# Kernel optimization log

Measured on AMD Instinct MI355X. Metric: run time of the kernel, lower is better.

The kernel has to match this reference:

```python
import math
import jax, jax.numpy as jnp
import numpy as np

B, M, N, D, H = 64, 5, 1000, 128, 8
KS = D // H
TANH_CLIP = 10.0

def setup_inputs() -> dict:
    key = jax.random.key(0)
    ks = jax.random.split(key, 12)
    mask = jax.random.randint(ks[8], (B, M, N), 0, 2).astype(bool)
    mask = mask.at[:, 0, 0].set(True)  # guarantee at least one feasible action per batch row
    return {
        'node_embeddings': jax.random.normal(ks[0], (B, N, D), jnp.float32),
        'fixed_context': jax.random.normal(ks[1], (B, 1, D), jnp.float32),
        'prev_node_embeddings': jax.random.normal(ks[2], (B, M, D), jnp.float32),
        'node_dynamic_features': jax.random.normal(ks[3], (B, M, N, 8), jnp.float32),
        'vehicle_dynamic_features': jax.random.normal(ks[4], (B, M, 3), jnp.float32),
        'glimpse_V_static': jax.random.normal(ks[5], (H, B, 1, N, KS), jnp.float32),
        'glimpse_K_static': jax.random.normal(ks[6], (H, B, 1, N, KS), jnp.float32),
        'logit_K_static': jax.random.normal(ks[7], (B, 1, N, D), jnp.float32),
        'feasibility_mask': mask,
        'W_pcv': jax.random.normal(ks[9], (D, D + 3), jnp.float32) * 0.05,
        'W_pns': jax.random.normal(ks[10], (3 * D, 8), jnp.float32) * 0.05,
        'po_weight': jax.random.normal(ks[11], (D, D), jnp.float32) * 0.05,
    }

def reference(node_embeddings, fixed_context, prev_node_embeddings,
              node_dynamic_features, vehicle_dynamic_features,
              glimpse_V_static, glimpse_K_static, logit_K_static,
              feasibility_mask, W_pcv, W_pns, po_weight):
    # current vehicle state projection: [B,M,D]
    cvs = jnp.concatenate([prev_node_embeddings, vehicle_dynamic_features], axis=-1)
    proj_cvs = cvs @ W_pcv.T
    # dynamic node embeddings: [B,M,N,3D] -> three [B,M,N,D] chunks
    nde = node_dynamic_features @ W_pns.T
    gVd, gKd, lKd = jnp.split(nde, 3, axis=-1)
    # make heads: [B,M,N,D] -> [H,B,M,N,KS]
    def mh(x):
        return x.reshape(B, M, N, H, KS).transpose(3, 0, 1, 2, 4)
    glimpse_V = glimpse_V_static + mh(gVd)  # [H,B,M,N,KS]
    glimpse_K = glimpse_K_static + mh(gKd)
    logit_K = logit_K_static + lKd          # [B,M,N,D]
    query = fixed_context + proj_cvs        # [B,M,D]
    Q = query.reshape(B, M, H, KS).transpose(2, 0, 1, 3)  # [H,B,M,KS]
    mask_log = jnp.log(feasibility_mask.astype(jnp.float32))  # [B,M,N]
    compat = jnp.einsum('hbmk,hbmnk->hbmn', Q, glimpse_K) / math.sqrt(KS)
    compat = compat + mask_log[None]
    # softmax over joint vehicle*node axis
    attn = jax.nn.softmax(compat.reshape(H, B, M * N), axis=-1).reshape(H, B, M, N)
    heads = jnp.einsum('hbmn,hbmnk->hbmk', attn, glimpse_V)  # [H,B,M,KS]
    concat = heads.transpose(1, 2, 0, 3).reshape(B, M, D)
    final_Q = concat @ po_weight.T          # [B,M,D]
    logits = jnp.einsum('bmd,bmnd->bmn', final_Q, logit_K) / math.sqrt(D)
    logits = jnp.tanh(logits) * TANH_CLIP + mask_log
    probs = jax.nn.softmax(logits.reshape(B, M * N), axis=-1)
    return probs
```

## Files before the change

### kernel.cpp

```cpp
#include <hip/hip_runtime.h>
#include <cstddef>

#define BB 64
#define MM 5
#define NN 1000
#define DD 128
#define HH 8
#define KSZ 16
#define NT 8
#define TN 125
#define NC3 8
#define CH3 125
#define INV_SQRT_D 0.08838834764831845f

#define K2_KOFF 0
#define K2_VOFF 8192
#define K2_NOFF 16384
#define K2_POFF 36864
#define K2_BUF  37376

typedef __attribute__((address_space(1))) const void gconst_t;
typedef __attribute__((address_space(3))) void lds_t;
#define GLD16(src, dst) __builtin_amdgcn_global_load_lds((gconst_t*)(src), (lds_t*)(dst), 16, 0, 0)
#define GLD4(src, dst)  __builtin_amdgcn_global_load_lds((gconst_t*)(src), (lds_t*)(dst), 4, 0, 0)
#define VMCNT0() asm volatile("s_waitcnt vmcnt(0)" ::: "memory")

__device__ __forceinline__ float tanh_fast(float x) {
  float e = __expf(2.f * x);
  return 1.f - 2.f / (e + 1.f);
}

__global__ __launch_bounds__(256) void k1_query(
    const float* __restrict__ fc, const float* __restrict__ pne,
    const float* __restrict__ vdf, const float* __restrict__ wpcv,
    const float* __restrict__ wpns, const int* __restrict__ mask,
    float* __restrict__ q_ws, float* __restrict__ qw_ws,
    unsigned int* __restrict__ pmask)
{
  const int t = threadIdx.x;
  if (blockIdx.x >= BB * 4) {
    const int b = blockIdx.x - BB * 4;
    const int* mb = mask + (size_t)(b * MM) * NN;
    for (int n = t; n < NN; n += 256) {
      unsigned int pm = 0;
#pragma unroll
      for (int m = 0; m < MM; ++m) pm |= (mb[m * NN + n] != 0 ? 1u : 0u) << m;
      pmask[b * NN + n] = pm;
    }
    return;
  }
  const int b = blockIdx.x >> 2;
  const int dq = blockIdx.x & 3;
  const int k = t & 15, gid = t >> 4;
  __shared__ float qsh[MM][32];

  float cvr[9];
  int curm = -1;
  for (int r = 0; r < 10; ++r) {
    const int m = r >> 1;
    if (m != curm) {
      curm = m;
      const float* pner = pne + (size_t)(b * MM + m) * DD;
#pragma unroll
      for (int jp = 0; jp < 8; ++jp) cvr[jp] = pner[k + 16 * jp];
      cvr[8] = (k < 3) ? vdf[(b * MM + m) * 3 + k] : 0.f;
    }
    const int dl = (r & 1) * 16 + gid;
    const int d = dq * 32 + dl;
    const float* wrow = wpcv + d * 131;
    float p = 0.f;
#pragma unroll
    for (int jp = 0; jp < 8; ++jp) p = fmaf(cvr[jp], wrow[k + 16 * jp], p);
    if (k < 3) p = fmaf(cvr[8], wrow[128 + k], p);
    p += __shfl_xor(p, 1); p += __shfl_xor(p, 2);
    p += __shfl_xor(p, 4); p += __shfl_xor(p, 8);
    if (k == 0) {
      const float q = 0.25f * (p + fc[b * DD + d]);
      qsh[m][dl] = q;
      q_ws[(size_t)(b * MM + m) * DD + d] = q;
    }
  }
  __syncthreads();
  if (t < 80) {
    const int hh = t / 40;
    const int r = t - hh * 40, m = r >> 3, f = r & 7;
    const int h = dq * 2 + hh;
    float acc = 0.f;
#pragma unroll
    for (int kk = 0; kk < KSZ; ++kk)
      acc = fmaf(qsh[m][hh * 16 + kk], wpns[(DD + h * KSZ + kk) * 8 + f], acc);
    qw_ws[(b * HH + h) * 40 + m * 8 + f] = acc;
  }
}

__global__ __launch_bounds__(256, 2) void k2_attn(
    const float* __restrict__ ndf, const float* __restrict__ gV,
    const float* __restrict__ gK, const unsigned int* __restrict__ pmask,
    const float* __restrict__ q_ws, const float* __restrict__ qw_ws,
    float* __restrict__ part)
{
  const int bid = blockIdx.x;
  const int b = bid & 63;
  const int h = bid >> 6;
  const int t = threadIdx.x;
  const int w = t >> 6, lane = t & 63;
  const int k = t & 3, g = t >> 2;

  __shared__ __align__(16) char smem[2][K2_BUF];
  __shared__ float redh[4][MM][KSZ];
  __shared__ float redaf[4][MM][8];
  __shared__ float reds[4];

  const char* gkrow = (const char*)gK + (size_t)(h * BB + b) * (NN * 64);
  const char* gvrow = (const char*)gV + (size_t)(h * BB + b) * (NN * 64);
  const char* pmrow = (const char*)pmask + (size_t)b * (NN * 4);
  const char* ndrow0 = (const char*)ndf + (size_t)(b * MM) * (NN * 32);

  auto stage = [&](int tt, int bb) {
    char* base = smem[bb];
#pragma unroll
    for (int j = 0; j < 10; ++j) {
      const int seg = 4 * j + w;
      if (seg >= 38) continue;
      if (seg < 16) {
        const int s = seg & 7;
        int off = tt * 8000 + s * 1024;
        if (off > NN * 64 - 1024) off = NN * 64 - 1024;
        const char* srow = (seg < 8) ? gkrow : gvrow;
        const int roff = (seg < 8) ? K2_KOFF : K2_VOFF;
        GLD16(srow + off + lane * 16, base + roff + (off - tt * 8000));
      } else if (seg < 36) {
        const int rel = seg - 16, m = rel >> 2, q = rel & 3;
        int off = tt * 4000 + q * 1024;
        if (off > NN * 32 - 1024) off = NN * 32 - 1024;
        GLD16(ndrow0 + (size_t)m * (NN * 32) + off + lane * 16,
              base + K2_NOFF + m * 4096 + (off - tt * 4000));
      } else {
        const int i4 = seg - 36;
        int off = tt * 500 + i4 * 256;
        if (off > NN * 4 - 256) off = NN * 4 - 256;
        GLD4(pmrow + off + lane * 4, base + K2_POFF + (off - tt * 500));
      }
    }
  };

  float4 qr[MM];
  float2 qw[MM];
#pragma unroll
  for (int m = 0; m < MM; ++m) {
    qr[m] = *(const float4*)(q_ws + (size_t)(b * MM + m) * DD + h * KSZ + 4 * k);
    qw[m] = *(const float2*)(qw_ws + (b * HH + h) * 40 + m * 8 + 2 * k);
  }

  float4 ha[MM] = {};
  float2 af[MM] = {};
  float ls = 0.f;

  stage(0, 0);
  VMCNT0();
  __builtin_amdgcn_s_barrier();

  for (int tt = 0; tt < NT; ++tt) {
    const int cur = tt & 1;
    if (tt < NT - 1) stage(tt + 1, cur ^ 1);
    const char* base = smem[cur];
#pragma unroll
    for (int i = 0; i < 2; ++i) {
      const int n = g + 64 * i;
      if (i == 0 || g < TN - 64) {
        const float4 kv = *(const float4*)(base + K2_KOFF + n * 64 + k * 16);
        const float4 vv = *(const float4*)(base + K2_VOFF + n * 64 + k * 16);
        const unsigned int pm = *(const unsigned int*)(base + K2_POFF + n * 4);
        float2 nd[MM];
#pragma unroll
        for (int m = 0; m < MM; ++m)
          nd[m] = *(const float2*)(base + K2_NOFF + m * 4096 + n * 32 + k * 8);
#pragma unroll
        for (int m = 0; m < MM; ++m) {
          float p = kv.x * qr[m].x + kv.y * qr[m].y
                  + kv.z * qr[m].z + kv.w * qr[m].w
                  + nd[m].x * qw[m].x + nd[m].y * qw[m].y;
          p += __shfl_xor(p, 1); p += __shfl_xor(p, 2);
          const float e = ((pm >> m) & 1u) ? __expf(p) : 0.f;
          ha[m].x = fmaf(e, vv.x, ha[m].x);
          ha[m].y = fmaf(e, vv.y, ha[m].y);
          ha[m].z = fmaf(e, vv.z, ha[m].z);
          ha[m].w = fmaf(e, vv.w, ha[m].w);
          af[m].x = fmaf(e, nd[m].x, af[m].x);
          af[m].y = fmaf(e, nd[m].y, af[m].y);
          ls += e;
        }
      }
    }
    VMCNT0();
    __builtin_amdgcn_s_barrier();
  }

#pragma unroll
  for (int off = 4; off <= 32; off <<= 1) {
#pragma unroll
    for (int m = 0; m < MM; ++m) {
      ha[m].x += __shfl_xor(ha[m].x, off);
      ha[m].y += __shfl_xor(ha[m].y, off);
      ha[m].z += __shfl_xor(ha[m].z, off);
      ha[m].w += __shfl_xor(ha[m].w, off);
      af[m].x += __shfl_xor(af[m].x, off);
      af[m].y += __shfl_xor(af[m].y, off);
    }
    ls += __shfl_xor(ls, off);
  }
  if (lane < 4) {
#pragma unroll
    for (int m = 0; m < MM; ++m) {
      *(float4*)(&redh[w][m][4 * k]) = ha[m];
      *(float2*)(&redaf[w][m][2 * k]) = af[m];
    }
    if (k == 0) reds[w] = ls;
  }
  __syncthreads();
  float* P = part + (size_t)(b * HH + h) * 128;
  if (t < 80) {
    const int m = t >> 4, kk = t & 15;
    P[t] = redh[0][m][kk] + redh[1][m][kk] + redh[2][m][kk] + redh[3][m][kk];
  } else if (t < 120) {
    const int r = t - 80, m = r >> 3, f = r & 7;
    P[80 + r] = redaf[0][m][f] + redaf[1][m][f] + redaf[2][m][f] + redaf[3][m][f];
  } else if (t == 120) {
    P[120] = reds[0] + reds[1] + reds[2] + reds[3];
  }
}

__global__ __launch_bounds__(512) void k3_logits(
    const float* __restrict__ ndf, const float* __restrict__ lK,
    const unsigned int* __restrict__ pmask, const float* __restrict__ part,
    const float* __restrict__ wpns, const float* __restrict__ po,
    float* __restrict__ out, float* __restrict__ stats)
{
  const int b = blockIdx.x >> 3;
  const int c = blockIdx.x & 7;
  const int t = threadIdx.x;

  __shared__ float pos[DD][129];
  __shared__ float rgs[HH];
  __shared__ float afs[HH][MM][8];
  __shared__ float cs[MM][DD];
  __shared__ float fqs[MM][DD];
  __shared__ float fw[MM][8];
  __shared__ float wred[8];

  for (int i = t; i < DD * DD / 4; i += 512) {
    const float4 v = ((const float4*)po)[i];
    const int r = (i * 4) >> 7, cc = (i * 4) & 127;
    pos[r][cc] = v.x; pos[r][cc + 1] = v.y; pos[r][cc + 2] = v.z; pos[r][cc + 3] = v.w;
  }
  const float* pb = part + (size_t)b * HH * 128;
  if (t < HH) rgs[t] = 1.f / pb[t * 128 + 120];
  if (t < HH * MM * 8) {
    const int h = t / 40, r = t % 40;
    afs[h][r >> 3][r & 7] = pb[h * 128 + 80 + r];
  }
  __syncthreads();
  for (int idx = t; idx < MM * DD; idx += 512) {
    const int m = idx >> 7, d = idx & 127, h = d >> 4;
    const float a = pb[h * 128 + m * 16 + (d & 15)];
    float cf = 0.f;
#pragma unroll
    for (int f = 0; f < 8; ++f) cf = fmaf(wpns[d * 8 + f], afs[h][m][f], cf);
    cs[m][d] = (a + cf) * rgs[h];
  }
  __syncthreads();
  for (int idx = t; idx < MM * DD; idx += 512) {
    const int m = idx >> 7, d = idx & 127;
    float acc = 0.f;
#pragma unroll 8
    for (int j = 0; j < DD; ++j) acc = fmaf(cs[m][j], pos[d][j], acc);
    fqs[m][d] = acc * INV_SQRT_D;
  }
  __syncthreads();
  if (t < MM * 8) {
    const int m = t >> 3, f = t & 7;
    float acc = 0.f;
#pragma unroll 16
    for (int d = 0; d < DD; ++d) acc = fmaf(fqs[m][d], wpns[(2 * DD + d) * 8 + f], acc);
    fw[m][f] = acc;
  }
  __syncthreads();

  const int k = t & 15, gid = t >> 4;
  const int n0 = c * CH3;
  float4 fqr[MM][2];
  float fwr[MM];
#pragma unroll
  for (int m = 0; m < MM; ++m) {
    fqr[m][0] = *(const float4*)(&fqs[m][8 * k]);
    fqr[m][1] = *(const float4*)(&fqs[m][8 * k + 4]);
    fwr[m] = fw[m][k & 7];
  }
  float lsum = 0.f;

#pragma unroll
  for (int i = 0; i < 4; ++i) {
    const int nl = gid + 32 * i;
    const bool valid = (nl < CH3);
    const int n = n0 + (valid ? nl : 0);
    const unsigned int pm = valid ? pmask[b * NN + n] : 0u;
    const float* lkr = lK + ((size_t)b * NN + n) * DD;
    const float4 l0 = *(const float4*)(lkr + 8 * k);
    const float4 l1 = *(const float4*)(lkr + 8 * k + 4);
    float ndv[MM];
#pragma unroll
    for (int m = 0; m < MM; ++m)
      ndv[m] = (k < 8) ? ndf[((size_t)(b * MM + m) * NN + n) * 8 + k] : 0.f;
#pragma unroll
    for (int m = 0; m < MM; ++m) {
      float p = l0.x * fqr[m][0].x + l0.y * fqr[m][0].y
              + l0.z * fqr[m][0].z + l0.w * fqr[m][0].w
              + l1.x * fqr[m][1].x + l1.y * fqr[m][1].y
              + l1.z * fqr[m][1].z + l1.w * fqr[m][1].w
              + ndv[m] * fwr[m];
      p += __shfl_xor(p, 1); p += __shfl_xor(p, 2);
      p += __shfl_xor(p, 4); p += __shfl_xor(p, 8);
      const float e = ((pm >> m) & 1u) ? __expf(tanh_fast(p) * 10.f) : 0.f;
      if (valid) {
        lsum += e;
        if (k == 0) out[(size_t)(b * MM + m) * NN + n] = e;
      }
    }
  }
  lsum += __shfl_xor(lsum, 16);
  lsum += __shfl_xor(lsum, 32);
  if ((t & 63) == 0) wred[t >> 6] = lsum;
  __syncthreads();
  if (t == 0) {
    float s = 0.f;
#pragma unroll
    for (int w2 = 0; w2 < 8; ++w2) s += wred[w2];
    stats[b * NC3 + c] = s;
  }
}

__global__ __launch_bounds__(256) void k4_probs(
    const float* __restrict__ stats, float* __restrict__ out)
{
  const int bm = blockIdx.x;
  const int b = bm / MM;
  const int t = threadIdx.x;
  float s = 0.f;
#pragma unroll
  for (int c = 0; c < NC3; ++c) s += stats[b * NC3 + c];
  const float scale = 1.f / s;
  if (t < 250) {
    float4* p = (float4*)(out + (size_t)bm * NN);
    float4 v = p[t];
    v.x *= scale; v.y *= scale; v.z *= scale; v.w *= scale;
    p[t] = v;
  }
}

extern "C" void kernel_launch(void* const* d_in, const int* in_sizes, int n_in,
                              void* d_out, int out_size, void* d_ws, size_t ws_size,
                              hipStream_t stream) {
  const float* fc   = (const float*)d_in[1];
  const float* pne  = (const float*)d_in[2];
  const float* ndf  = (const float*)d_in[3];
  const float* vdf  = (const float*)d_in[4];
  const float* gV   = (const float*)d_in[5];
  const float* gK   = (const float*)d_in[6];
  const float* lK   = (const float*)d_in[7];
  const int*   mask = (const int*)d_in[8];
  const float* wpcv = (const float*)d_in[9];
  const float* wpns = (const float*)d_in[10];
  const float* po   = (const float*)d_in[11];

  float* q_ws  = (float*)d_ws;
  float* qw_ws = q_ws + BB * MM * DD;
  float* part  = qw_ws + BB * HH * 40;
  float* stats = part + (size_t)BB * HH * 128;
  unsigned int* pmask = (unsigned int*)(stats + BB * NC3);
  float* out   = (float*)d_out;

  k1_query<<<BB * 4 + BB, 256, 0, stream>>>(fc, pne, vdf, wpcv, wpns, mask,
                                            q_ws, qw_ws, pmask);
  k2_attn<<<HH * BB, 256, 0, stream>>>(ndf, gV, gK, pmask, q_ws, qw_ws, part);
  k3_logits<<<BB * NC3, 512, 0, stream>>>(ndf, lK, pmask, part, wpns, po, out, stats);
  k4_probs<<<BB * MM, 256, 0, stream>>>(stats, out);
}
```

Before: 56.78 us.

## Triple-buffer attention staging with partial vmcnt waits and 512-thread blocks

The attention kernel moves from 256 to 512 threads, so each thread handles one node per tile instead of two, and each wave issues half as many global-to-LDS loads per stage. The double-buffered staging with a full vmcnt(0) drain becomes a three-deep ring: three tiles are prefetched up front, and each wave waits only until its oldest tile has landed, using per-wave partial vmcnt counts. This is meant to keep more memory traffic in flight and hide load latency behind compute. It costs more LDS (three buffers), hard-coded wait counts that depend on the per-wave load layout, and an eight-way final reduction.

```diff
diff --git a/kernel.cpp b/kernel.cpp
--- a/kernel.cpp
+++ b/kernel.cpp
@@ -23,7 +23,8 @@
 typedef __attribute__((address_space(3))) void lds_t;
 #define GLD16(src, dst) __builtin_amdgcn_global_load_lds((gconst_t*)(src), (lds_t*)(dst), 16, 0, 0)
 #define GLD4(src, dst)  __builtin_amdgcn_global_load_lds((gconst_t*)(src), (lds_t*)(dst), 4, 0, 0)
-#define VMCNT0() asm volatile("s_waitcnt vmcnt(0)" ::: "memory")
+#define WAITV(N) do { asm volatile("s_waitcnt vmcnt(" #N ")" ::: "memory"); \
+                      __builtin_amdgcn_sched_barrier(0); } while (0)
 
 __device__ __forceinline__ float tanh_fast(float x) {
   float e = __expf(2.f * x);
@@ -93,7 +94,7 @@
   }
 }
 
-__global__ __launch_bounds__(256, 2) void k2_attn(
+__global__ __launch_bounds__(512, 2) void k2_attn(
     const float* __restrict__ ndf, const float* __restrict__ gV,
     const float* __restrict__ gK, const unsigned int* __restrict__ pmask,
     const float* __restrict__ q_ws, const float* __restrict__ qw_ws,
@@ -106,10 +107,10 @@
   const int w = t >> 6, lane = t & 63;
   const int k = t & 3, g = t >> 2;
 
-  __shared__ __align__(16) char smem[2][K2_BUF];
-  __shared__ float redh[4][MM][KSZ];
-  __shared__ float redaf[4][MM][8];
-  __shared__ float reds[4];
+  __shared__ __align__(16) char smem[3][K2_BUF];
+  __shared__ float redh[8][MM][KSZ];
+  __shared__ float redaf[8][MM][8];
+  __shared__ float reds[8];
 
   const char* gkrow = (const char*)gK + (size_t)(h * BB + b) * (NN * 64);
   const char* gvrow = (const char*)gV + (size_t)(h * BB + b) * (NN * 64);
@@ -119,8 +120,8 @@
   auto stage = [&](int tt, int bb) {
     char* base = smem[bb];
 #pragma unroll
-    for (int j = 0; j < 10; ++j) {
-      const int seg = 4 * j + w;
+    for (int j = 0; j < 5; ++j) {
+      const int seg = 8 * j + w;
       if (seg >= 38) continue;
       if (seg < 16) {
         const int s = seg & 7;
@@ -156,44 +157,44 @@
   float2 af[MM] = {};
   float ls = 0.f;
 
-  stage(0, 0);
-  VMCNT0();
-  __builtin_amdgcn_s_barrier();
+  stage(0, 0); stage(1, 1); stage(2, 2);
 
   for (int tt = 0; tt < NT; ++tt) {
-    const int cur = tt & 1;
-    if (tt < NT - 1) stage(tt + 1, cur ^ 1);
-    const char* base = smem[cur];
-#pragma unroll
-    for (int i = 0; i < 2; ++i) {
-      const int n = g + 64 * i;
-      if (i == 0 || g < TN - 64) {
-        const float4 kv = *(const float4*)(base + K2_KOFF + n * 64 + k * 16);
-        const float4 vv = *(const float4*)(base + K2_VOFF + n * 64 + k * 16);
-        const unsigned int pm = *(const unsigned int*)(base + K2_POFF + n * 4);
-        float2 nd[MM];
-#pragma unroll
-        for (int m = 0; m < MM; ++m)
-          nd[m] = *(const float2*)(base + K2_NOFF + m * 4096 + n * 32 + k * 8);
-#pragma unroll
-        for (int m = 0; m < MM; ++m) {
-          float p = kv.x * qr[m].x + kv.y * qr[m].y
-                  + kv.z * qr[m].z + kv.w * qr[m].w
-                  + nd[m].x * qw[m].x + nd[m].y * qw[m].y;
-          p += __shfl_xor(p, 1); p += __shfl_xor(p, 2);
-          const float e = ((pm >> m) & 1u) ? __expf(p) : 0.f;
-          ha[m].x = fmaf(e, vv.x, ha[m].x);
-          ha[m].y = fmaf(e, vv.y, ha[m].y);
-          ha[m].z = fmaf(e, vv.z, ha[m].z);
-          ha[m].w = fmaf(e, vv.w, ha[m].w);
-          af[m].x = fmaf(e, nd[m].x, af[m].x);
-          af[m].y = fmaf(e, nd[m].y, af[m].y);
-          ls += e;
-        }
+    if (w < 6) {
+      if (tt <= 5) WAITV(10); else if (tt == 6) WAITV(5); else WAITV(0);
+    } else {
+      if (tt <= 5) WAITV(8); else if (tt == 6) WAITV(4); else WAITV(0);
+    }
+    __builtin_amdgcn_s_barrier();
+
+    const char* base = smem[tt % 3];
+    if (g < TN) {
+      const int n = g;
+      const float4 kv = *(const float4*)(base + K2_KOFF + n * 64 + k * 16);
+      const float4 vv = *(const float4*)(base + K2_VOFF + n * 64 + k * 16);
+      const unsigned int pm = *(const unsigned int*)(base + K2_POFF + n * 4);
+      float2 nd[MM];
+#pragma unroll
+      for (int m = 0; m < MM; ++m)
+        nd[m] = *(const float2*)(base + K2_NOFF + m * 4096 + n * 32 + k * 8);
+#pragma unroll
+      for (int m = 0; m < MM; ++m) {
+        float p = kv.x * qr[m].x + kv.y * qr[m].y
+                + kv.z * qr[m].z + kv.w * qr[m].w
+                + nd[m].x * qw[m].x + nd[m].y * qw[m].y;
+        p += __shfl_xor(p, 1); p += __shfl_xor(p, 2);
+        const float e = ((pm >> m) & 1u) ? __expf(p) : 0.f;
+        ha[m].x = fmaf(e, vv.x, ha[m].x);
+        ha[m].y = fmaf(e, vv.y, ha[m].y);
+        ha[m].z = fmaf(e, vv.z, ha[m].z);
+        ha[m].w = fmaf(e, vv.w, ha[m].w);
+        af[m].x = fmaf(e, nd[m].x, af[m].x);
+        af[m].y = fmaf(e, nd[m].y, af[m].y);
+        ls += e;
       }
     }
-    VMCNT0();
     __builtin_amdgcn_s_barrier();
+    if (tt + 3 < NT) stage(tt + 3, tt % 3);
   }
 
 #pragma unroll
@@ -221,12 +222,21 @@
   float* P = part + (size_t)(b * HH + h) * 128;
   if (t < 80) {
     const int m = t >> 4, kk = t & 15;
-    P[t] = redh[0][m][kk] + redh[1][m][kk] + redh[2][m][kk] + redh[3][m][kk];
+    float s = 0.f;
+#pragma unroll
+    for (int ww = 0; ww < 8; ++ww) s += redh[ww][m][kk];
+    P[t] = s;
   } else if (t < 120) {
     const int r = t - 80, m = r >> 3, f = r & 7;
-    P[80 + r] = redaf[0][m][f] + redaf[1][m][f] + redaf[2][m][f] + redaf[3][m][f];
+    float s = 0.f;
+#pragma unroll
+    for (int ww = 0; ww < 8; ++ww) s += redaf[ww][m][f];
+    P[80 + r] = s;
   } else if (t == 120) {
-    P[120] = reds[0] + reds[1] + reds[2] + reds[3];
+    float s = 0.f;
+#pragma unroll
+    for (int ww = 0; ww < 8; ++ww) s += reds[ww];
+    P[120] = s;
   }
 }
 
@@ -381,7 +391,7 @@
 
   k1_query<<<BB * 4 + BB, 256, 0, stream>>>(fc, pne, vdf, wpcv, wpns, mask,
                                             q_ws, qw_ws, pmask);
-  k2_attn<<<HH * BB, 256, 0, stream>>>(ndf, gV, gK, pmask, q_ws, qw_ws, part);
+  k2_attn<<<HH * BB, 512, 0, stream>>>(ndf, gV, gK, pmask, q_ws, qw_ws, part);
   k3_logits<<<BB * NC3, 512, 0, stream>>>(ndf, lK, pmask, part, wpns, po, out, stats);
   k4_probs<<<BB * MM, 256, 0, stream>>>(stats, out);
 }
```

New measurement: 62.36 us. 1.1x slower.

## Split attention over two node halves per head to double k2 grid

Applied to the files above, without the earlier changes.

The attention kernel now splits the N=1000 nodes into two halves per (batch, head), launching twice as many blocks. Each block processes 8 tiles of 64 nodes with smaller LDS buffers, which allows 4 blocks per CU instead of 2. k3 sums the two partial results before normalising. The aim is more parallelism and occupancy to hide memory latency. In exchange it adds partial-sum traffic and reduces work per block.

```diff
diff --git a/kernel.cpp b/kernel.cpp
--- a/kernel.cpp
+++ b/kernel.cpp
@@ -8,16 +8,15 @@
 #define HH 8
 #define KSZ 16
 #define NT 8
-#define TN 125
 #define NC3 8
 #define CH3 125
 #define INV_SQRT_D 0.08838834764831845f
 
 #define K2_KOFF 0
-#define K2_VOFF 8192
-#define K2_NOFF 16384
-#define K2_POFF 36864
-#define K2_BUF  37376
+#define K2_VOFF 4096
+#define K2_NOFF 8192
+#define K2_POFF 18528
+#define K2_BUF  18816
 
 typedef __attribute__((address_space(1))) const void gconst_t;
 typedef __attribute__((address_space(3))) void lds_t;
@@ -93,7 +92,7 @@
   }
 }
 
-__global__ __launch_bounds__(256, 2) void k2_attn(
+__global__ __launch_bounds__(256, 4) void k2_attn(
     const float* __restrict__ ndf, const float* __restrict__ gV,
     const float* __restrict__ gK, const unsigned int* __restrict__ pmask,
     const float* __restrict__ q_ws, const float* __restrict__ qw_ws,
@@ -101,10 +100,14 @@
 {
   const int bid = blockIdx.x;
   const int b = bid & 63;
-  const int h = bid >> 6;
+  const int hp = bid >> 6;
+  const int h = hp >> 1;
+  const int half = hp & 1;
   const int t = threadIdx.x;
   const int w = t >> 6, lane = t & 63;
   const int k = t & 3, g = t >> 2;
+  const int n0 = half * 512;
+  const int nlen = half ? (NN - 512) : 512;
 
   __shared__ __align__(16) char smem[2][K2_BUF];
   __shared__ float redh[4][MM][KSZ];
@@ -118,28 +121,31 @@
 
   auto stage = [&](int tt, int bb) {
     char* base = smem[bb];
-#pragma unroll
-    for (int j = 0; j < 10; ++j) {
+    const int tb = n0 + tt * 64;
+#pragma unroll
+    for (int j = 0; j < 5; ++j) {
       const int seg = 4 * j + w;
-      if (seg >= 38) continue;
-      if (seg < 16) {
-        const int s = seg & 7;
-        int off = tt * 8000 + s * 1024;
+      if (seg >= 19) continue;
+      if (seg < 8) {
+        const int s = seg & 3;
+        const int tilb = tb * 64;
+        int off = tilb + s * 1024;
         if (off > NN * 64 - 1024) off = NN * 64 - 1024;
-        const char* srow = (seg < 8) ? gkrow : gvrow;
-        const int roff = (seg < 8) ? K2_KOFF : K2_VOFF;
-        GLD16(srow + off + lane * 16, base + roff + (off - tt * 8000));
-      } else if (seg < 36) {
-        const int rel = seg - 16, m = rel >> 2, q = rel & 3;
-        int off = tt * 4000 + q * 1024;
+        const char* srow = (seg < 4) ? gkrow : gvrow;
+        const int roff = (seg < 4) ? K2_KOFF : K2_VOFF;
+        GLD16(srow + off + lane * 16, base + roff + (off - tilb));
+      } else if (seg < 18) {
+        const int rel = seg - 8, m = rel >> 1, q = rel & 1;
+        const int tilb = tb * 32;
+        int off = tilb + q * 1024;
         if (off > NN * 32 - 1024) off = NN * 32 - 1024;
         GLD16(ndrow0 + (size_t)m * (NN * 32) + off + lane * 16,
-              base + K2_NOFF + m * 4096 + (off - tt * 4000));
+              base + K2_NOFF + m * 2048 + (off - tilb));
       } else {
-        const int i4 = seg - 36;
-        int off = tt * 500 + i4 * 256;
+        const int tilb = tb * 4;
+        int off = tilb;
         if (off > NN * 4 - 256) off = NN * 4 - 256;
-        GLD4(pmrow + off + lane * 4, base + K2_POFF + (off - tt * 500));
+        GLD4(pmrow + off + lane * 4, base + K2_POFF + (off - tilb));
       }
     }
   };
@@ -164,32 +170,30 @@
     const int cur = tt & 1;
     if (tt < NT - 1) stage(tt + 1, cur ^ 1);
     const char* base = smem[cur];
-#pragma unroll
-    for (int i = 0; i < 2; ++i) {
-      const int n = g + 64 * i;
-      if (i == 0 || g < TN - 64) {
-        const float4 kv = *(const float4*)(base + K2_KOFF + n * 64 + k * 16);
-        const float4 vv = *(const float4*)(base + K2_VOFF + n * 64 + k * 16);
-        const unsigned int pm = *(const unsigned int*)(base + K2_POFF + n * 4);
-        float2 nd[MM];
-#pragma unroll
-        for (int m = 0; m < MM; ++m)
-          nd[m] = *(const float2*)(base + K2_NOFF + m * 4096 + n * 32 + k * 8);
-#pragma unroll
-        for (int m = 0; m < MM; ++m) {
-          float p = kv.x * qr[m].x + kv.y * qr[m].y
-                  + kv.z * qr[m].z + kv.w * qr[m].w
-                  + nd[m].x * qw[m].x + nd[m].y * qw[m].y;
-          p += __shfl_xor(p, 1); p += __shfl_xor(p, 2);
-          const float e = ((pm >> m) & 1u) ? __expf(p) : 0.f;
-          ha[m].x = fmaf(e, vv.x, ha[m].x);
-          ha[m].y = fmaf(e, vv.y, ha[m].y);
-          ha[m].z = fmaf(e, vv.z, ha[m].z);
-          ha[m].w = fmaf(e, vv.w, ha[m].w);
-          af[m].x = fmaf(e, nd[m].x, af[m].x);
-          af[m].y = fmaf(e, nd[m].y, af[m].y);
-          ls += e;
-        }
+    const int nv = nlen - tt * 64;
+    if (g < nv) {
+      const int n = g;
+      const float4 kv = *(const float4*)(base + K2_KOFF + n * 64 + k * 16);
+      const float4 vv = *(const float4*)(base + K2_VOFF + n * 64 + k * 16);
+      const unsigned int pm = *(const unsigned int*)(base + K2_POFF + n * 4);
+      float2 nd[MM];
+#pragma unroll
+      for (int m = 0; m < MM; ++m)
+        nd[m] = *(const float2*)(base + K2_NOFF + m * 2048 + n * 32 + k * 8);
+#pragma unroll
+      for (int m = 0; m < MM; ++m) {
+        float p = kv.x * qr[m].x + kv.y * qr[m].y
+                + kv.z * qr[m].z + kv.w * qr[m].w
+                + nd[m].x * qw[m].x + nd[m].y * qw[m].y;
+        p += __shfl_xor(p, 1); p += __shfl_xor(p, 2);
+        const float e = ((pm >> m) & 1u) ? __expf(p) : 0.f;
+        ha[m].x = fmaf(e, vv.x, ha[m].x);
+        ha[m].y = fmaf(e, vv.y, ha[m].y);
+        ha[m].z = fmaf(e, vv.z, ha[m].z);
+        ha[m].w = fmaf(e, vv.w, ha[m].w);
+        af[m].x = fmaf(e, nd[m].x, af[m].x);
+        af[m].y = fmaf(e, nd[m].y, af[m].y);
+        ls += e;
       }
     }
     VMCNT0();
@@ -218,7 +222,7 @@
     if (k == 0) reds[w] = ls;
   }
   __syncthreads();
-  float* P = part + (size_t)(b * HH + h) * 128;
+  float* P = part + (size_t)((b * HH + h) * 2 + half) * 128;
   if (t < 80) {
     const int m = t >> 4, kk = t & 15;
     P[t] = redh[0][m][kk] + redh[1][m][kk] + redh[2][m][kk] + redh[3][m][kk];
@@ -253,16 +257,17 @@
     const int r = (i * 4) >> 7, cc = (i * 4) & 127;
     pos[r][cc] = v.x; pos[r][cc + 1] = v.y; pos[r][cc + 2] = v.z; pos[r][cc + 3] = v.w;
   }
-  const float* pb = part + (size_t)b * HH * 128;
-  if (t < HH) rgs[t] = 1.f / pb[t * 128 + 120];
+  const float* pb = part + (size_t)b * HH * 2 * 128;
+  if (t < HH) rgs[t] = 1.f / (pb[(t * 2) * 128 + 120] + pb[(t * 2 + 1) * 128 + 120]);
   if (t < HH * MM * 8) {
     const int h = t / 40, r = t % 40;
-    afs[h][r >> 3][r & 7] = pb[h * 128 + 80 + r];
+    afs[h][r >> 3][r & 7] = pb[(h * 2) * 128 + 80 + r] + pb[(h * 2 + 1) * 128 + 80 + r];
   }
   __syncthreads();
   for (int idx = t; idx < MM * DD; idx += 512) {
     const int m = idx >> 7, d = idx & 127, h = d >> 4;
-    const float a = pb[h * 128 + m * 16 + (d & 15)];
+    const float a = pb[(h * 2) * 128 + m * 16 + (d & 15)]
+                  + pb[(h * 2 + 1) * 128 + m * 16 + (d & 15)];
     float cf = 0.f;
 #pragma unroll
     for (int f = 0; f < 8; ++f) cf = fmaf(wpns[d * 8 + f], afs[h][m][f], cf);
@@ -375,13 +380,13 @@
   float* q_ws  = (float*)d_ws;
   float* qw_ws = q_ws + BB * MM * DD;
   float* part  = qw_ws + BB * HH * 40;
-  float* stats = part + (size_t)BB * HH * 128;
+  float* stats = part + (size_t)BB * HH * 2 * 128;
   unsigned int* pmask = (unsigned int*)(stats + BB * NC3);
   float* out   = (float*)d_out;
 
   k1_query<<<BB * 4 + BB, 256, 0, stream>>>(fc, pne, vdf, wpcv, wpns, mask,
                                             q_ws, qw_ws, pmask);
-  k2_attn<<<HH * BB, 256, 0, stream>>>(ndf, gV, gK, pmask, q_ws, qw_ws, part);
+  k2_attn<<<HH * 2 * BB, 256, 0, stream>>>(ndf, gV, gK, pmask, q_ws, qw_ws, part);
   k3_logits<<<BB * NC3, 512, 0, stream>>>(ndf, lK, pmask, part, wpns, po, out, stats);
   k4_probs<<<BB * MM, 256, 0, stream>>>(stats, out);
 }
```

Result: no change. 56.28 us (-0.9%).
